# Performance work log

Measured on AMD Instinct MI355X. Metric: run time of the kernel, lower is better.

## Reference

```python
import jax, jax.numpy as jnp
import numpy as np

WS = 8        # window_size
NH = 8        # num_heads
LN_EPS = 1e-5

# static relative-position index table [WS*WS, WS*WS], values in [0, (2*WS-1)**2)
def _rel_index(ws):
    coords = np.arange(ws)
    grid = np.stack(np.meshgrid(coords, coords, indexing='ij')).reshape(2, -1)  # [2, W2]
    rel = grid[:, :, None] - grid[:, None, :]            # [2, W2, W2]
    rel = rel.transpose(1, 2, 0).copy()                   # [W2, W2, 2]
    rel[..., 0] += ws - 1
    rel[..., 1] += ws - 1
    rel[..., 0] *= 2 * ws - 1
    return rel.sum(-1)                                    # [W2, W2]

REL_IDX = jnp.asarray(_rel_index(WS))


def _ln(x):
    # LayerNorm without affine params (elementwise_affine=False)
    mu = jnp.mean(x, axis=-1, keepdims=True)
    var = jnp.var(x, axis=-1, keepdims=True)
    return (x - mu) * jax.lax.rsqrt(var + LN_EPS)


def setup_inputs() -> dict:
    key = jax.random.key(0)
    ks = jax.random.split(key, 16)
    B, Hg, Wg, C = 8, 64, 64, 256
    L = Hg * Wg
    s = 0.02
    inp = {
        'x': jax.random.normal(ks[0], (B, L, C), jnp.float32),
        't_embed': jax.random.normal(ks[1], (B, C), jnp.float32),
        'H': Hg,
        'W': Wg,
        'adaln1_w': s * jax.random.normal(ks[2], (C, 2 * C), jnp.float32),
        'adaln1_b': jnp.zeros((2 * C,), jnp.float32),
        'adaln2_w': s * jax.random.normal(ks[3], (C, 2 * C), jnp.float32),
        'adaln2_b': jnp.zeros((2 * C,), jnp.float32),
        'bias_table': s * jax.random.normal(ks[4], ((2 * WS - 1) ** 2, NH), jnp.float32),
        'q_w': s * jax.random.normal(ks[5], (C, C), jnp.float32),
        'q_b': jnp.zeros((C,), jnp.float32),
        'k_w': s * jax.random.normal(ks[6], (C, C), jnp.float32),
        'k_b': jnp.zeros((C,), jnp.float32),
        'v_w': s * jax.random.normal(ks[7], (C, C), jnp.float32),
        'v_b': jnp.zeros((C,), jnp.float32),
        'o_w': s * jax.random.normal(ks[8], (C, C), jnp.float32),
        'o_b': jnp.zeros((C,), jnp.float32),
        'ffn1_w': s * jax.random.normal(ks[9], (C, 4 * C), jnp.float32),
        'ffn1_b': jnp.zeros((4 * C,), jnp.float32),
        'ffn2_w': s * jax.random.normal(ks[10], (4 * C, C), jnp.float32),
        'ffn2_b': jnp.zeros((C,), jnp.float32),
    }
    return inp


def reference(x, t_embed, H, W, adaln1_w, adaln1_b, adaln2_w, adaln2_b,
              bias_table, q_w, q_b, k_w, k_b, v_w, v_b, o_w, o_b,
              ffn1_w, ffn1_b, ffn2_w, ffn2_b):
    B, L, C = x.shape
    d = C // NH
    W2 = WS * WS
    sh = WS // 2  # cyclic shift (shifted=True)

    # --- AdaLN1 ---
    ss = t_embed @ adaln1_w + adaln1_b              # [B, 2C]
    scale, shift = jnp.split(ss, 2, axis=-1)
    xn = _ln(x) * (1.0 + scale[:, None, :]) + shift[:, None, :]

    # --- shifted window partition ---
    xg = xn.reshape(B, H, W, C)
    xg = jnp.roll(xg, (-sh, -sh), axis=(1, 2))
    xw = xg.reshape(B, H // WS, WS, W // WS, WS, C).transpose(0, 1, 3, 2, 4, 5)
    xw = xw.reshape(-1, W2, C)                       # [nwB, W2, C]
    nwB = xw.shape[0]

    # --- window attention with relative position bias ---
    q = (xw @ q_w + q_b).reshape(nwB, W2, NH, d).transpose(0, 2, 1, 3)
    k = (xw @ k_w + k_b).reshape(nwB, W2, NH, d).transpose(0, 2, 1, 3)
    v = (xw @ v_w + v_b).reshape(nwB, W2, NH, d).transpose(0, 2, 1, 3)
    logits = jnp.einsum('whqd,whkd->whqk', q, k) * (d ** -0.5)
    bias = bias_table[REL_IDX.reshape(-1)].reshape(W2, W2, NH).transpose(2, 0, 1)
    logits = logits + bias[None].astype(logits.dtype)
    attn = jax.nn.softmax(logits, axis=-1)
    out = jnp.einsum('whqk,whkd->whqd', attn, v).transpose(0, 2, 1, 3).reshape(nwB, W2, C)
    out = out @ o_w + o_b

    # --- window reverse + unshift ---
    xm = out.reshape(B, H // WS, W // WS, WS, WS, C).transpose(0, 1, 3, 2, 4, 5)
    xm = xm.reshape(B, H, W, C)
    xm = jnp.roll(xm, (sh, sh), axis=(1, 2))
    x = x + xm.reshape(B, L, C)

    # --- AdaLN2 + FFN (GELU exact, matching torch nn.GELU) ---
    ss2 = t_embed @ adaln2_w + adaln2_b
    sc2, sh2 = jnp.split(ss2, 2, axis=-1)
    xn2 = _ln(x) * (1.0 + sc2[:, None, :]) + sh2[:, None, :]
    h = jax.nn.gelu(xn2 @ ffn1_w + ffn1_b, approximate=False)
    x = x + (h @ ffn2_w + ffn2_b)
    return x
```

## Files before the change

kernel.cpp:

```cpp
#include <hip/hip_runtime.h>
#include <math.h>

#define WS_ 8
#define NH_ 8
#define C_ 256
#define B_ 8
#define M_ 32768
#define SH_ 4
#define LN_EPS 1e-5f
#define SL_ 8388608

typedef __attribute__((ext_vector_type(8))) short bf16x8;
typedef __attribute__((ext_vector_type(4))) float f32x4;

__device__ inline float b2f(unsigned short u) {
    union { unsigned int i; float f; } c; c.i = ((unsigned int)u) << 16; return c.f;
}
__device__ inline unsigned short f2b(float f) {
    union { unsigned int i; float f; } c; c.f = f;
    unsigned int u = c.i;
    return (unsigned short)((u + 0x7FFFu + ((u >> 16) & 1u)) >> 16);
}
__device__ inline float gelu_f(float x) {
    float t = 1.59576912160573f * (x + 0.044715f * x * x * x);
    return x / (1.f + __expf(-t));
}

__global__ void prep_k(const float* __restrict__ qw, const float* __restrict__ kw,
                       const float* __restrict__ vw, const float* __restrict__ ow,
                       const float* __restrict__ f1w, const float* __restrict__ f2w,
                       const float* __restrict__ qb, const float* __restrict__ kb,
                       const float* __restrict__ vb, const float* __restrict__ bt,
                       const float* __restrict__ te,
                       const float* __restrict__ a1w, const float* __restrict__ a1b,
                       const float* __restrict__ a2w, const float* __restrict__ a2b,
                       unsigned short* __restrict__ qkvT, unsigned short* __restrict__ oT,
                       unsigned short* __restrict__ f1T, unsigned short* __restrict__ f2T,
                       float* __restrict__ qkvB, float* __restrict__ bias_full,
                       float* __restrict__ ss1, float* __restrict__ ss2) {
    int t = blockIdx.x * 256 + threadIdx.x;
    if (t < 196608) {
        int n = t >> 8, k = t & 255;
        const float* w = n < 256 ? qw : (n < 512 ? kw : vw);
        qkvT[t] = f2b(w[k * 256 + (n & 255)]);
    } else if (t < 262144) {
        int i = t - 196608; int n = i >> 8, k = i & 255;
        oT[i] = f2b(ow[k * 256 + n]);
    } else if (t < 524288) {
        int i = t - 262144; int n = i >> 8, k = i & 255;
        f1T[i] = f2b(f1w[k * 1024 + n]);
    } else if (t < 786432) {
        int i = t - 524288; int n = i >> 10, k = i & 1023;
        f2T[i] = f2b(f2w[k * 256 + n]);
    } else if (t < 787200) {
        int i = t - 786432;
        qkvB[i] = i < 256 ? qb[i] : (i < 512 ? kb[i - 256] : vb[i - 512]);
    } else if (t < 819968) {
        int i = t - 787200;
        int head = i >> 12, qk = i & 4095;
        int q = qk >> 6, k = qk & 63;
        int qh = q >> 3, qw2 = q & 7, kh = k >> 3, kw2 = k & 7;
        bias_full[i] = bt[((qh - kh + 7) * 15 + (qw2 - kw2 + 7)) * 8 + head];
    } else if (t < 828160) {
        int i = t - 819968;
        int which = i >> 12;
        int rem = i & 4095;
        int b = rem >> 9, col = rem & 511;
        const float* w = which ? a2w : a1w;
        const float* bb = which ? a2b : a1b;
        const float* tr = te + b * C_;
        float acc = bb[col];
        for (int k = 0; k < C_; ++k) acc += tr[k] * w[k * 512 + col];
        (which ? ss2 : ss1)[b * 512 + col] = acc;
    }
}

__global__ __launch_bounds__(256) void ln_win_k(const float* __restrict__ x,
                                                const float* __restrict__ ss,
                                                unsigned short* __restrict__ xw) {
    int t = blockIdx.x * 4 + (threadIdx.x >> 6);
    int lane = threadIdx.x & 63;
    int b = t >> 12, rem = t & 4095;
    int hg = rem >> 6, wg = rem & 63;
    int hs = (hg + SH_) & 63, wsrc = (wg + SH_) & 63;
    size_t src = ((size_t)b << 12) + (hs << 6) + wsrc;
    float4 v = *(const float4*)&x[src * C_ + lane * 4];
    float s = v.x + v.y + v.z + v.w;
    float s2 = v.x * v.x + v.y * v.y + v.z * v.z + v.w * v.w;
#pragma unroll
    for (int m = 1; m < 64; m <<= 1) { s += __shfl_xor(s, m); s2 += __shfl_xor(s2, m); }
    float mu = s * (1.f / 256.f);
    float rstd = rsqrtf(s2 * (1.f / 256.f) - mu * mu + LN_EPS);
    float4 sc = *(const float4*)&ss[b * 512 + lane * 4];
    float4 sh = *(const float4*)&ss[b * 512 + 256 + lane * 4];
    int win = (b << 6) + ((hg >> 3) << 3) + (wg >> 3);
    int pos = ((hg & 7) << 3) + (wg & 7);
    ushort4 pk;
    pk.x = f2b((v.x - mu) * rstd * (1.f + sc.x) + sh.x);
    pk.y = f2b((v.y - mu) * rstd * (1.f + sc.y) + sh.y);
    pk.z = f2b((v.z - mu) * rstd * (1.f + sc.z) + sh.z);
    pk.w = f2b((v.w - mu) * rstd * (1.f + sc.w) + sh.w);
    *(ushort4*)(xw + (size_t)(win * 64 + pos) * C_ + lane * 4) = pk;
}

template <int KDIM, int MODE, int NT, int MINW>
__global__ __launch_bounds__(256, MINW) void gemm_bf16_k(
    const unsigned short* __restrict__ A, const unsigned short* __restrict__ Bt,
    const float* __restrict__ bias, const float* __restrict__ res,
    void* __restrict__ Cout, int Nout) {
    __shared__ __align__(16) unsigned short As[2][4096];
    const int blk = blockIdx.x;
    const int xcd = blk & 7;
    const int idx = blk >> 3;
    const int mt = xcd + ((idx / NT) << 3);
    const int nt = idx % NT;
    const int bm = mt * 128, bn = nt * 128;
    const int tid = threadIdx.x;
    const int w = tid >> 6, lane = tid & 63;
    const int quad = lane >> 4, l16 = lane & 15;
    const int wm = (w >> 1) * 64, wn = (w & 1) * 64;
    const int srow = lane >> 2;
    const int qlog = ((lane & 3) ^ ((lane >> 3) & 3)) << 3;
    const int rsw = ((l16 >> 1) & 3) << 3;

    f32x4 acc[4][4] = {};
    const unsigned short* bp = Bt + (size_t)(bn + wn + l16) * KDIM + quad * 8;

    for (int k0 = 0; k0 < KDIM; k0 += 64) {
        if (k0) __syncthreads();
#pragma unroll
        for (int h = 0; h < 2; ++h) {
#pragma unroll
            for (int j = 0; j < 2; ++j) {
                int r = j * 64 + w * 16 + srow;
                const unsigned short* ga = A + (size_t)(bm + r) * KDIM + k0 + h * 32 + qlog;
                unsigned short* la = &As[h][j * 2048 + w * 512 + lane * 8];
                __builtin_amdgcn_global_load_lds(
                    (const __attribute__((address_space(1))) void*)ga,
                    (__attribute__((address_space(3))) void*)la, 16, 0, 0);
            }
        }
        __syncthreads();
#pragma unroll
        for (int h = 0; h < 2; ++h) {
            bf16x8 af[4], bfr[4];
#pragma unroll
            for (int j = 0; j < 4; ++j)
                bfr[j] = *(const bf16x8*)(bp + (size_t)j * 16 * KDIM + k0 + h * 32);
#pragma unroll
            for (int i = 0; i < 4; ++i)
                af[i] = *(const bf16x8*)&As[h][(wm + i * 16 + l16) * 32 + ((quad << 3) ^ rsw)];
#pragma unroll
            for (int i = 0; i < 4; ++i)
#pragma unroll
                for (int j = 0; j < 4; ++j)
                    acc[i][j] = __builtin_amdgcn_mfma_f32_16x16x32_bf16(
                        bfr[j], af[i], acc[i][j], 0, 0, 0);
        }
    }

    if constexpr (MODE == 0 || MODE == 2) {
        unsigned short* bb = &As[0][0];
#pragma unroll
        for (int half = 0; half < 2; ++half) {
            __syncthreads();
            if ((w >> 1) == half) {
#pragma unroll
                for (int i = 0; i < 4; ++i) {
                    const int lr = i * 16 + l16;
#pragma unroll
                    for (int j = 0; j < 4; ++j) {
                        const int lc = wn + j * 16 + quad * 4;
                        float4 bv = *(const float4*)&bias[bn + lc];
                        float v0 = acc[i][j][0] + bv.x, v1 = acc[i][j][1] + bv.y;
                        float v2 = acc[i][j][2] + bv.z, v3 = acc[i][j][3] + bv.w;
                        ushort4 pk;
                        if (MODE == 2) {
                            pk.x = f2b(gelu_f(v0)); pk.y = f2b(gelu_f(v1));
                            pk.z = f2b(gelu_f(v2)); pk.w = f2b(gelu_f(v3));
                        } else {
                            pk.x = f2b(v0); pk.y = f2b(v1);
                            pk.z = f2b(v2); pk.w = f2b(v3);
                        }
                        int sw = (lc >> 3) ^ (lr & 7);
                        *(ushort4*)&bb[lr * 128 + sw * 8 + (lc & 7)] = pk;
                    }
                }
            }
            __syncthreads();
#pragma unroll
            for (int s = 0; s < 4; ++s) {
                int iidx = s * 256 + tid;
                int lr = iidx >> 4, c16 = iidx & 15;
                bf16x8 v = *(const bf16x8*)&bb[lr * 128 + ((c16 ^ (lr & 7)) * 8)];
                const int grow = bm + half * 64 + lr;
                if (MODE == 2) {
                    *(bf16x8*)((unsigned short*)Cout + (size_t)grow * Nout +
                               bn + c16 * 8) = v;
                } else {
                    int win = grow >> 6, pos = grow & 63;
                    int col = bn + c16 * 8;
                    int which = col >> 8, head = (col >> 5) & 7, dc = col & 31;
                    *(bf16x8*)((unsigned short*)Cout + (size_t)which * SL_ +
                               (size_t)win * 16384 + pos * 32 + head * 2048 + dc) = v;
                }
            }
        }
    } else {
#pragma unroll
        for (int i = 0; i < 4; ++i) {
            const int row = bm + wm + i * 16 + l16;
            size_t rowbase = (size_t)row * Nout;
#pragma unroll
            for (int j = 0; j < 4; ++j) {
                const int col = bn + wn + j * 16 + quad * 4;
                float4 bv = *(const float4*)&bias[col];
                float v0 = acc[i][j][0] + bv.x, v1 = acc[i][j][1] + bv.y;
                float v2 = acc[i][j][2] + bv.z, v3 = acc[i][j][3] + bv.w;
                float4 rv = *(const float4*)&res[rowbase + col];
                float4 ov = {v0 + rv.x, v1 + rv.y, v2 + rv.z, v3 + rv.w};
                *(float4*)&((float*)Cout)[rowbase + col] = ov;
            }
        }
    }
}

__global__ __launch_bounds__(256, 4) void oproj_ln_k(
    const unsigned short* __restrict__ A, const unsigned short* __restrict__ Bt,
    const float* __restrict__ bias, const float* __restrict__ res,
    float* __restrict__ x1, const float* __restrict__ ss2,
    unsigned short* __restrict__ xn2) {
    __shared__ __align__(16) unsigned short As[2][64 * 32];
    __shared__ __align__(16) unsigned short Bs[2][256 * 32];
    const int bm = blockIdx.x * 64;
    const int tid = threadIdx.x;
    const int w = tid >> 6, lane = tid & 63;
    const int quad = lane >> 4, l16 = lane & 15;
    const int wn = w * 64;
    const int srow = lane >> 2;
    const int qlog = ((lane & 3) ^ ((lane >> 3) & 3)) << 3;
    const int rsw = ((l16 >> 1) & 3) << 3;

    f32x4 acc[4][4] = {};

    for (int k0 = 0; k0 < 256; k0 += 64) {
        if (k0) __syncthreads();
#pragma unroll
        for (int h = 0; h < 2; ++h) {
            {
                int r = w * 16 + srow;
                const unsigned short* ga = A + (size_t)(bm + r) * 256 + k0 + h * 32 + qlog;
                __builtin_amdgcn_global_load_lds(
                    (const __attribute__((address_space(1))) void*)ga,
                    (__attribute__((address_space(3))) void*)&As[h][w * 512 + lane * 8],
                    16, 0, 0);
            }
#pragma unroll
            for (int j = 0; j < 4; ++j) {
                int r = j * 64 + w * 16 + srow;
                const unsigned short* gb = Bt + (size_t)r * 256 + k0 + h * 32 + qlog;
                __builtin_amdgcn_global_load_lds(
                    (const __attribute__((address_space(1))) void*)gb,
                    (__attribute__((address_space(3))) void*)
                        &Bs[h][j * 2048 + w * 512 + lane * 8], 16, 0, 0);
            }
        }
        __syncthreads();
#pragma unroll
        for (int h = 0; h < 2; ++h) {
            bf16x8 af[4], bfr[4];
#pragma unroll
            for (int i = 0; i < 4; ++i)
                af[i] = *(const bf16x8*)&As[h][(i * 16 + l16) * 32 + ((quad << 3) ^ rsw)];
#pragma unroll
            for (int j = 0; j < 4; ++j)
                bfr[j] = *(const bf16x8*)&Bs[h][(wn + j * 16 + l16) * 32 + ((quad << 3) ^ rsw)];
#pragma unroll
            for (int i = 0; i < 4; ++i)
#pragma unroll
                for (int j = 0; j < 4; ++j)
                    acc[i][j] = __builtin_amdgcn_mfma_f32_16x16x32_bf16(
                        bfr[j], af[i], acc[i][j], 0, 0, 0);
        }
    }

    float ps[4], ps2[4];
#pragma unroll
    for (int i = 0; i < 4; ++i) {
        const int row = bm + i * 16 + l16;
        int win = row >> 6, pos = row & 63;
        int b = win >> 6, wh = (win >> 3) & 7, ww = win & 7;
        int hg = (wh << 3) + (pos >> 3), wg = (ww << 3) + (pos & 7);
        int hd = (hg + SH_) & 63, wd = (wg + SH_) & 63;
        size_t rowbase = (((size_t)b << 12) + (hd << 6) + wd) * C_;
        float s = 0.f, s2 = 0.f;
#pragma unroll
        for (int j = 0; j < 4; ++j) {
            const int col = wn + j * 16 + quad * 4;
            float4 bv = *(const float4*)&bias[col];
            float4 rv = *(const float4*)&res[rowbase + col];
            float4 ov = {acc[i][j][0] + bv.x + rv.x, acc[i][j][1] + bv.y + rv.y,
                         acc[i][j][2] + bv.z + rv.z, acc[i][j][3] + bv.w + rv.w};
            *(float4*)&x1[rowbase + col] = ov;
            acc[i][j][0] = ov.x; acc[i][j][1] = ov.y;
            acc[i][j][2] = ov.z; acc[i][j][3] = ov.w;
            s += ov.x + ov.y + ov.z + ov.w;
            s2 += ov.x * ov.x + ov.y * ov.y + ov.z * ov.z + ov.w * ov.w;
        }
        ps[i] = s; ps2[i] = s2;
    }
#pragma unroll
    for (int i = 0; i < 4; ++i) {
        ps[i] += __shfl_xor(ps[i], 16);  ps[i] += __shfl_xor(ps[i], 32);
        ps2[i] += __shfl_xor(ps2[i], 16); ps2[i] += __shfl_xor(ps2[i], 32);
    }
    float* sred = (float*)&As[0][0];
    __syncthreads();
    if (quad == 0) {
#pragma unroll
        for (int i = 0; i < 4; ++i) {
            int r = i * 16 + l16;
            sred[(w * 64 + r) * 2 + 0] = ps[i];
            sred[(w * 64 + r) * 2 + 1] = ps2[i];
        }
    }
    __syncthreads();
#pragma unroll
    for (int i = 0; i < 4; ++i) {
        int r = i * 16 + l16;
        float s = 0.f, s2 = 0.f;
#pragma unroll
        for (int cw = 0; cw < 4; ++cw) {
            s  += sred[(cw * 64 + r) * 2 + 0];
            s2 += sred[(cw * 64 + r) * 2 + 1];
        }
        float mu = s * (1.f / 256.f);
        float rstd = rsqrtf(s2 * (1.f / 256.f) - mu * mu + LN_EPS);
        const int row = bm + i * 16 + l16;
        int win = row >> 6, pos = row & 63;
        int b = win >> 6, wh = (win >> 3) & 7, ww = win & 7;
        int hg = (wh << 3) + (pos >> 3), wg = (ww << 3) + (pos & 7);
        int hd = (hg + SH_) & 63, wd = (wg + SH_) & 63;
        size_t rowbase = (((size_t)b << 12) + (hd << 6) + wd) * C_;
#pragma unroll
        for (int j = 0; j < 4; ++j) {
            const int col = wn + j * 16 + quad * 4;
            float4 scv = *(const float4*)&ss2[b * 512 + col];
            float4 shv = *(const float4*)&ss2[b * 512 + 256 + col];
            ushort4 pk;
            pk.x = f2b((acc[i][j][0] - mu) * rstd * (1.f + scv.x) + shv.x);
            pk.y = f2b((acc[i][j][1] - mu) * rstd * (1.f + scv.y) + shv.y);
            pk.z = f2b((acc[i][j][2] - mu) * rstd * (1.f + scv.z) + shv.z);
            pk.w = f2b((acc[i][j][3] - mu) * rstd * (1.f + scv.w) + shv.w);
            *(ushort4*)(xn2 + rowbase + col) = pk;
        }
    }
}

__global__ __launch_bounds__(256) void attn_mfma_k(
    const unsigned short* __restrict__ qkv, const float* __restrict__ bias_full,
    unsigned short* __restrict__ attn_out) {
    __shared__ __align__(16) unsigned short Pb[4][64 * 66];
    __shared__ __align__(16) unsigned short Vt[4][32 * 66];
    const int w = threadIdx.x >> 6, lane = threadIdx.x & 63;
    const int wh = blockIdx.x * 4 + w;
    const int win = wh >> 3, head = wh & 7;
    const int quad = lane >> 4, l16 = lane & 15;

    const unsigned short* qp = qkv + (size_t)win * 16384 + head * 2048;
    const unsigned short* kp = qp + SL_;
    const unsigned short* vp = qp + 2 * (size_t)SL_;

    {
        const uint4* v4 = (const uint4*)(vp + lane * 32);
        unsigned short* dst = &Vt[w][0];
#pragma unroll
        for (int c = 0; c < 4; ++c) {
            uint4 u = v4[c];
            unsigned int uu[4] = {u.x, u.y, u.z, u.w};
#pragma unroll
            for (int p = 0; p < 4; ++p) {
                int d0 = c * 8 + p * 2;
                dst[d0 * 66 + lane] = (unsigned short)(uu[p] & 0xffff);
                dst[(d0 + 1) * 66 + lane] = (unsigned short)(uu[p] >> 16);
            }
        }
    }

    bf16x8 qf[4], kf[4];
#pragma unroll
    for (int i = 0; i < 4; ++i) {
        qf[i] = *(const bf16x8*)(qp + (i * 16 + l16) * 32 + quad * 8);
        kf[i] = *(const bf16x8*)(kp + (i * 16 + l16) * 32 + quad * 8);
    }

    f32x4 s[4][4] = {};
#pragma unroll
    for (int i = 0; i < 4; ++i)
#pragma unroll
        for (int j = 0; j < 4; ++j)
            s[i][j] = __builtin_amdgcn_mfma_f32_16x16x32_bf16(qf[i], kf[j], s[i][j], 0, 0, 0);

    const float scale = 0.17677669529663687f;
    const float* bf = bias_full + head * 4096;
    float rs[4][4];
#pragma unroll
    for (int i = 0; i < 4; ++i) {
#pragma unroll
        for (int r = 0; r < 4; ++r) {
            int row = i * 16 + quad * 4 + r;
            float acc = 0.f;
#pragma unroll
            for (int j = 0; j < 4; ++j) {
                float e = __expf(s[i][j][r] * scale + bf[row * 64 + j * 16 + l16]);
                s[i][j][r] = e;
                acc += e;
            }
#pragma unroll
            for (int msk = 1; msk < 16; msk <<= 1) acc += __shfl_xor(acc, msk);
            rs[i][r] = 1.f / acc;
        }
    }

#pragma unroll
    for (int i = 0; i < 4; ++i)
#pragma unroll
        for (int j = 0; j < 4; ++j)
#pragma unroll
            for (int r = 0; r < 4; ++r)
                Pb[w][(i * 16 + quad * 4 + r) * 66 + j * 16 + l16] = f2b(s[i][j][r]);

    __syncthreads();

    f32x4 o[4][2] = {};
#pragma unroll
    for (int st = 0; st < 2; ++st) {
        bf16x8 bv[2];
#pragma unroll
        for (int jo = 0; jo < 2; ++jo)
            bv[jo] = *(const bf16x8*)&Vt[w][(jo * 16 + l16) * 66 + st * 32 + quad * 8];
#pragma unroll
        for (int i = 0; i < 4; ++i) {
            bf16x8 af = *(const bf16x8*)&Pb[w][(i * 16 + l16) * 66 + st * 32 + quad * 8];
#pragma unroll
            for (int jo = 0; jo < 2; ++jo)
                o[i][jo] = __builtin_amdgcn_mfma_f32_16x16x32_bf16(af, bv[jo], o[i][jo], 0, 0, 0);
        }
    }

#pragma unroll
    for (int i = 0; i < 4; ++i)
#pragma unroll
        for (int jo = 0; jo < 2; ++jo)
#pragma unroll
            for (int r = 0; r < 4; ++r) {
                int row = i * 16 + quad * 4 + r;
                int d = jo * 16 + l16;
                attn_out[((size_t)(win * 64 + row)) * C_ + head * 32 + d] =
                    f2b(o[i][jo][r] * rs[i][r]);
            }
}

extern "C" void kernel_launch(void* const* d_in, const int* in_sizes, int n_in,
                              void* d_out, int out_size, void* d_ws, size_t ws_size,
                              hipStream_t stream) {
    const float* x        = (const float*)d_in[0];
    const float* t_embed  = (const float*)d_in[1];
    const float* adaln1_w = (const float*)d_in[4];
    const float* adaln1_b = (const float*)d_in[5];
    const float* adaln2_w = (const float*)d_in[6];
    const float* adaln2_b = (const float*)d_in[7];
    const float* bt       = (const float*)d_in[8];
    const float* q_w = (const float*)d_in[9],  *q_b = (const float*)d_in[10];
    const float* k_w = (const float*)d_in[11], *k_b = (const float*)d_in[12];
    const float* v_w = (const float*)d_in[13], *v_b = (const float*)d_in[14];
    const float* o_w = (const float*)d_in[15], *o_b = (const float*)d_in[16];
    const float* f1_w = (const float*)d_in[17], *f1_b = (const float*)d_in[18];
    const float* f2_w = (const float*)d_in[19], *f2_b = (const float*)d_in[20];
    float* out = (float*)d_out;

    char* wsb = (char*)d_ws;
    float* ss1            = (float*)(wsb + 0);
    float* ss2            = (float*)(wsb + 16384);
    float* qkvB           = (float*)(wsb + 32768);
    unsigned short* qkvT  = (unsigned short*)(wsb + 36864);
    unsigned short* oT    = (unsigned short*)(wsb + 430080);
    unsigned short* f1T   = (unsigned short*)(wsb + 561152);
    unsigned short* f2T   = (unsigned short*)(wsb + 1085440);
    float* bias_full      = (float*)(wsb + 1609728);
    unsigned short* xw    = (unsigned short*)(wsb + 2097152);
    unsigned short* qkv   = (unsigned short*)(wsb + 18874368);
    unsigned short* attn  = (unsigned short*)(wsb + 69206016);
    unsigned short* xn2   = xw;
    unsigned short* hbuf  = qkv;
    float* x1             = (float*)(wsb + 85983232);

    prep_k<<<3235, 256, 0, stream>>>(q_w, k_w, v_w, o_w, f1_w, f2_w, q_b, k_b, v_b, bt,
                                     t_embed, adaln1_w, adaln1_b, adaln2_w, adaln2_b,
                                     qkvT, oT, f1T, f2T, qkvB, bias_full, ss1, ss2);
    ln_win_k<<<8192, 256, 0, stream>>>(x, ss1, xw);

    gemm_bf16_k<256, 0, 6, 4><<<1536, 256, 0, stream>>>(xw, qkvT, qkvB, nullptr, qkv, 768);

    attn_mfma_k<<<1024, 256, 0, stream>>>(qkv, bias_full, attn);

    oproj_ln_k<<<512, 256, 0, stream>>>(attn, oT, o_b, x, x1, ss2, xn2);

    gemm_bf16_k<256, 2, 8, 4><<<2048, 256, 0, stream>>>(xn2, f1T, f1_b, nullptr, hbuf, 1024);
    gemm_bf16_k<1024, 3, 2, 4><<<512, 256, 0, stream>>>(hbuf, f2T, f2_b, x1, out, 256);
}
```

Before: 316.7 us.

## Stage B weight tiles through LDS in GEMM and widen epilogue staging

The GEMM kernel now stages the B (weight) tile into shared memory with async global-to-LDS loads, alongside A, instead of each wave reading B fragments directly from global memory. The shared buffer doubles to 32 KB, which lets the bf16 epilogue stage the full 128x128 output tile in one pass rather than two half passes, removing a sync round. Launch-bound minimum waves are lowered to match the larger LDS use. The trade-off is more LDS pressure and lower occupancy in exchange for fewer redundant global/L2 reads of B.

```diff
diff --git a/kernel.cpp b/kernel.cpp
--- a/kernel.cpp
+++ b/kernel.cpp
@@ -108,7 +108,9 @@
     const unsigned short* __restrict__ A, const unsigned short* __restrict__ Bt,
     const float* __restrict__ bias, const float* __restrict__ res,
     void* __restrict__ Cout, int Nout) {
-    __shared__ __align__(16) unsigned short As[2][4096];
+    __shared__ __align__(16) unsigned short smem[16384];
+    unsigned short (*As)[4096] = (unsigned short (*)[4096])&smem[0];
+    unsigned short (*Bs)[4096] = (unsigned short (*)[4096])&smem[8192];
     const int blk = blockIdx.x;
     const int xcd = blk & 7;
     const int idx = blk >> 3;
@@ -124,7 +126,6 @@
     const int rsw = ((l16 >> 1) & 3) << 3;
 
     f32x4 acc[4][4] = {};
-    const unsigned short* bp = Bt + (size_t)(bn + wn + l16) * KDIM + quad * 8;
 
     for (int k0 = 0; k0 < KDIM; k0 += 64) {
         if (k0) __syncthreads();
@@ -138,6 +139,11 @@
                 __builtin_amdgcn_global_load_lds(
                     (const __attribute__((address_space(1))) void*)ga,
                     (__attribute__((address_space(3))) void*)la, 16, 0, 0);
+                const unsigned short* gb = Bt + (size_t)(bn + r) * KDIM + k0 + h * 32 + qlog;
+                unsigned short* lb = &Bs[h][j * 2048 + w * 512 + lane * 8];
+                __builtin_amdgcn_global_load_lds(
+                    (const __attribute__((address_space(1))) void*)gb,
+                    (__attribute__((address_space(3))) void*)lb, 16, 0, 0);
             }
         }
         __syncthreads();
@@ -145,11 +151,11 @@
         for (int h = 0; h < 2; ++h) {
             bf16x8 af[4], bfr[4];
 #pragma unroll
-            for (int j = 0; j < 4; ++j)
-                bfr[j] = *(const bf16x8*)(bp + (size_t)j * 16 * KDIM + k0 + h * 32);
-#pragma unroll
             for (int i = 0; i < 4; ++i)
                 af[i] = *(const bf16x8*)&As[h][(wm + i * 16 + l16) * 32 + ((quad << 3) ^ rsw)];
+#pragma unroll
+            for (int j = 0; j < 4; ++j)
+                bfr[j] = *(const bf16x8*)&Bs[h][(wn + j * 16 + l16) * 32 + ((quad << 3) ^ rsw)];
 #pragma unroll
             for (int i = 0; i < 4; ++i)
 #pragma unroll
@@ -160,50 +166,42 @@
     }
 
     if constexpr (MODE == 0 || MODE == 2) {
-        unsigned short* bb = &As[0][0];
-#pragma unroll
-        for (int half = 0; half < 2; ++half) {
-            __syncthreads();
-            if ((w >> 1) == half) {
-#pragma unroll
-                for (int i = 0; i < 4; ++i) {
-                    const int lr = i * 16 + l16;
-#pragma unroll
-                    for (int j = 0; j < 4; ++j) {
-                        const int lc = wn + j * 16 + quad * 4;
-                        float4 bv = *(const float4*)&bias[bn + lc];
-                        float v0 = acc[i][j][0] + bv.x, v1 = acc[i][j][1] + bv.y;
-                        float v2 = acc[i][j][2] + bv.z, v3 = acc[i][j][3] + bv.w;
-                        ushort4 pk;
-                        if (MODE == 2) {
-                            pk.x = f2b(gelu_f(v0)); pk.y = f2b(gelu_f(v1));
-                            pk.z = f2b(gelu_f(v2)); pk.w = f2b(gelu_f(v3));
-                        } else {
-                            pk.x = f2b(v0); pk.y = f2b(v1);
-                            pk.z = f2b(v2); pk.w = f2b(v3);
-                        }
-                        int sw = (lc >> 3) ^ (lr & 7);
-                        *(ushort4*)&bb[lr * 128 + sw * 8 + (lc & 7)] = pk;
-                    }
+        __syncthreads();
+#pragma unroll
+        for (int i = 0; i < 4; ++i) {
+            const int lrow = wm + i * 16 + l16;
+#pragma unroll
+            for (int j = 0; j < 4; ++j) {
+                const int lcol = wn + j * 16 + quad * 4;
+                float4 bv = *(const float4*)&bias[bn + lcol];
+                float v0 = acc[i][j][0] + bv.x, v1 = acc[i][j][1] + bv.y;
+                float v2 = acc[i][j][2] + bv.z, v3 = acc[i][j][3] + bv.w;
+                ushort4 pk;
+                if (MODE == 2) {
+                    pk.x = f2b(gelu_f(v0)); pk.y = f2b(gelu_f(v1));
+                    pk.z = f2b(gelu_f(v2)); pk.w = f2b(gelu_f(v3));
+                } else {
+                    pk.x = f2b(v0); pk.y = f2b(v1); pk.z = f2b(v2); pk.w = f2b(v3);
                 }
-            }
-            __syncthreads();
-#pragma unroll
-            for (int s = 0; s < 4; ++s) {
-                int iidx = s * 256 + tid;
-                int lr = iidx >> 4, c16 = iidx & 15;
-                bf16x8 v = *(const bf16x8*)&bb[lr * 128 + ((c16 ^ (lr & 7)) * 8)];
-                const int grow = bm + half * 64 + lr;
-                if (MODE == 2) {
-                    *(bf16x8*)((unsigned short*)Cout + (size_t)grow * Nout +
-                               bn + c16 * 8) = v;
-                } else {
-                    int win = grow >> 6, pos = grow & 63;
-                    int col = bn + c16 * 8;
-                    int which = col >> 8, head = (col >> 5) & 7, dc = col & 31;
-                    *(bf16x8*)((unsigned short*)Cout + (size_t)which * SL_ +
-                               (size_t)win * 16384 + pos * 32 + head * 2048 + dc) = v;
-                }
+                int sw = (lcol >> 3) ^ (lrow & 7);
+                *(ushort4*)&smem[lrow * 128 + sw * 8 + (lcol & 7)] = pk;
+            }
+        }
+        __syncthreads();
+#pragma unroll
+        for (int p = 0; p < 8; ++p) {
+            const int lrow = p * 16 + (tid >> 4);
+            const int c16 = tid & 15;
+            bf16x8 v = *(const bf16x8*)&smem[lrow * 128 + ((c16 ^ (lrow & 7)) * 8)];
+            const int grow = bm + lrow;
+            if (MODE == 2) {
+                *(bf16x8*)((unsigned short*)Cout + (size_t)grow * Nout + bn + c16 * 8) = v;
+            } else {
+                int win = grow >> 6, pos = grow & 63;
+                int col = bn + c16 * 8;
+                int which = col >> 8, head = (col >> 5) & 7, dc = col & 31;
+                *(bf16x8*)((unsigned short*)Cout + (size_t)which * SL_ +
+                           (size_t)win * 16384 + pos * 32 + head * 2048 + dc) = v;
             }
         }
     } else {
@@ -500,12 +498,12 @@
                                      qkvT, oT, f1T, f2T, qkvB, bias_full, ss1, ss2);
     ln_win_k<<<8192, 256, 0, stream>>>(x, ss1, xw);
 
-    gemm_bf16_k<256, 0, 6, 4><<<1536, 256, 0, stream>>>(xw, qkvT, qkvB, nullptr, qkv, 768);
+    gemm_bf16_k<256, 0, 6, 3><<<1536, 256, 0, stream>>>(xw, qkvT, qkvB, nullptr, qkv, 768);
 
     attn_mfma_k<<<1024, 256, 0, stream>>>(qkv, bias_full, attn);
 
     oproj_ln_k<<<512, 256, 0, stream>>>(attn, oT, o_b, x, x1, ss2, xn2);
 
-    gemm_bf16_k<256, 2, 8, 4><<<2048, 256, 0, stream>>>(xn2, f1T, f1_b, nullptr, hbuf, 1024);
-    gemm_bf16_k<1024, 3, 2, 4><<<512, 256, 0, stream>>>(hbuf, f2T, f2_b, x1, out, 256);
-}
+    gemm_bf16_k<256, 2, 8, 3><<<2048, 256, 0, stream>>>(xn2, f1T, f1_b, nullptr, hbuf, 1024);
+    gemm_bf16_k<1024, 3, 2, 1><<<512, 256, 0, stream>>>(hbuf, f2T, f2_b, x1, out, 256);
+}
```

Measured after the change: 269.9 us. 14.8% less time.
